# Performance work log

Measured on AMD Instinct MI355X. Metric: run time of the kernel, lower is better.

Reference implementation:

```python
import jax, jax.numpy as jnp
import numpy as np

HEADS = 8
DIM_HEAD = 64
MAX_POS = 512


def setup_inputs() -> dict:
    key = jax.random.key(0)
    ks = jax.random.split(key, 10)
    b, n, dim, inner = 4, 1024, 512, HEADS * DIM_HEAD
    w = lambda k, shape: jax.random.normal(k, shape, jnp.float32) * 0.02
    return {
        "x": jax.random.normal(ks[0], (b, n, dim, 2), jnp.float32),
        "wq_r": w(ks[1], (dim, inner)),
        "wq_i": w(ks[2], (dim, inner)),
        "wkv_r": w(ks[3], (dim, 2 * inner)),
        "wkv_i": w(ks[4], (dim, 2 * inner)),
        "wo_r": w(ks[5], (inner, dim)),
        "wo_i": w(ks[6], (inner, dim)),
        "bo_r": w(ks[7], (dim,)),
        "bo_i": w(ks[8], (dim,)),
        "rel_emb": w(ks[9], (2 * MAX_POS + 1, DIM_HEAD)),
    }


def _clinear(t, Wr, Wi, br=None, bi=None):
    # complex linear: (a+ib)(Wr+iWi) = (aWr - bWi) + i(bWr + aWi)
    a, b = t[..., 0], t[..., 1]
    r = a @ Wr - b @ Wi
    i = b @ Wr + a @ Wi
    if br is not None:
        r = r + br
        i = i + bi
    return jnp.stack((r, i), axis=-1)


def _split_heads(t, h):
    # [b, n, h*d, 2] -> [b, h, n, d, 2]
    b, n, hd, c = t.shape
    return t.reshape(b, n, h, hd // h, c).transpose(0, 2, 1, 3, 4)


def reference(x, wq_r, wq_i, wkv_r, wkv_i, wo_r, wo_i, bo_r, bo_i, rel_emb):
    b, n = x.shape[0], x.shape[1]
    scale = DIM_HEAD ** (-0.5)

    q = _split_heads(_clinear(x, wq_r, wq_i), HEADS)          # [b,h,n,d,2]
    kv = _clinear(x, wkv_r, wkv_i)                            # [b,n,2*inner,2]
    k_, v_ = jnp.split(kv, 2, axis=-2)
    k = _split_heads(k_, HEADS)
    v = _split_heads(v_, HEADS)

    qr, qi = q[..., 0], q[..., 1]
    kr, ki = k[..., 0], k[..., 1]

    dots_r = (jnp.einsum('bhid,bhjd->bhij', qr, kr)
              - jnp.einsum('bhid,bhjd->bhij', qi, ki)) * scale
    dots_i = (jnp.einsum('bhid,bhjd->bhij', qr, ki)
              + jnp.einsum('bhid,bhjd->bhij', qi, kr)) * scale

    seq = jnp.arange(n)
    dist = jnp.clip(seq[:, None] - seq[None, :], -MAX_POS, MAX_POS) + MAX_POS  # [n,n]
    rel = rel_emb[dist]                                       # [n, n, d]
    dots_r = dots_r + jnp.einsum('bhnd,nrd->bhnr', qr, rel) * scale
    dots_i = dots_i + jnp.einsum('bhnd,nrd->bhnr', qi, rel) * scale

    # magnitude softmax over keys
    attn = jax.nn.softmax(jnp.sqrt(dots_r ** 2 + dots_i ** 2), axis=-1)  # [b,h,i,j]

    vr, vi = v[..., 0], v[..., 1]
    out_r = jnp.einsum('bhij,bhjd->bhid', attn, vr)
    out_i = jnp.einsum('bhij,bhjd->bhid', attn, vi)
    # [b,h,n,d] -> [b,n,h*d]
    out_r = out_r.transpose(0, 2, 1, 3).reshape(b, n, -1)
    out_i = out_i.transpose(0, 2, 1, 3).reshape(b, n, -1)
    out = jnp.stack((out_r, out_i), axis=-1)                  # [b,n,inner,2]

    # to_out (with bias); dropout prob 0 -> identity
    return _clinear(out, wo_r, wo_i, bo_r, bo_i)
```

## Files before the change

### kernel.cpp

```cpp
#include <hip/hip_runtime.h>
#include <hip/hip_bf16.h>


using bf16 = __bf16;
typedef __bf16 bf16x8 __attribute__((ext_vector_type(8)));
typedef float f32x4 __attribute__((ext_vector_type(4)));
typedef unsigned u32x4 __attribute__((ext_vector_type(4)));

#define MFMA16(a, b, c) __builtin_amdgcn_mfma_f32_16x16x32_bf16((a), (b), (c), 0, 0, 0)

__device__ __forceinline__ float ld_in(const void* p, long long i, int f32) {
  return f32 ? ((const float*)p)[i] : (float)((const bf16*)p)[i];
}

__device__ __forceinline__ void gl_lds16(const bf16* g, const bf16* l) {
  __builtin_amdgcn_global_load_lds(
      (const __attribute__((address_space(1))) void*)(unsigned long long)g,
      (__attribute__((address_space(3))) void*)(unsigned int)(unsigned long long)l,
      16, 0, 0);
}

template <int CTRL>
__device__ __forceinline__ float dpp_mv(float v) {
  int s = __builtin_bit_cast(int, v);
  return __builtin_bit_cast(float,
      __builtin_amdgcn_update_dpp(s, s, CTRL, 0xf, 0xf, false));
}
__device__ __forceinline__ float dpp_sum16(float v) {
  v += dpp_mv<0x121>(v);
  v += dpp_mv<0x122>(v);
  v += dpp_mv<0x124>(v);
  v += dpp_mv<0x128>(v);
  return v;
}

__device__ __forceinline__ unsigned pack_bf16(float lo, float hi) {
  unsigned a = (unsigned)__builtin_bit_cast(unsigned short, (bf16)lo);
  unsigned b = (unsigned)__builtin_bit_cast(unsigned short, (bf16)hi);
  return a | (b << 16);
}
__device__ __forceinline__ unsigned pack2h(bf16 lo, bf16 hi) {
  unsigned a = (unsigned)__builtin_bit_cast(unsigned short, lo);
  unsigned b = (unsigned)__builtin_bit_cast(unsigned short, hi);
  return a | (b << 16);
}

__global__ __launch_bounds__(256) void k_diag(float* __restrict__ out, float v) {
  int idx = blockIdx.x * 256 + threadIdx.x;
  if (idx < 4194304) out[idx] = v;
}

__global__ void k_detect_all(
    const unsigned short* p0, const unsigned short* p1, const unsigned short* p2,
    const unsigned short* p3, const unsigned short* p4, const unsigned short* p5,
    const unsigned short* p6, const unsigned short* p7, const unsigned short* p8,
    const unsigned short* p9, int* __restrict__ flags) {
  static const int sizes[10] = {65536, 65536, 65536, 65536, 65536,
                                65536, 65536, 512, 512, 65536};
  const unsigned short* ptrs[10] = {p0, p1, p2, p3, p4, p5, p6, p7, p8, p9};
  __shared__ int cnt;
  if (threadIdx.x == 0) cnt = 0;
  __syncthreads();
  const int which = blockIdx.x;
  const unsigned short* p = ptrs[which];
  const int nhalf = sizes[which];
  const int ns = nhalf < 4096 ? nhalf : 4096;
  const int stp = nhalf / ns;
  int c = 0;
  for (int i = threadIdx.x; i < ns; i += 256) {
    const unsigned u = p[(size_t)i * stp];
    const unsigned e = (u >> 7) & 0xFF;
    if (e == 0xFF || (e < 64 && (u & 0x7FFF) != 0)) ++c;
  }
  atomicAdd(&cnt, c);
  __syncthreads();
  if (threadIdx.x == 0) flags[which] = (cnt > (ns >> 6)) ? 1 : 0;
}

__global__ __launch_bounds__(256) void k_build_all(
    const void* __restrict__ x,
    const void* __restrict__ wq_r, const void* __restrict__ wq_i,
    const void* __restrict__ wkv_r, const void* __restrict__ wkv_i,
    const void* __restrict__ wo_r, const void* __restrict__ wo_i,
    const void* __restrict__ rel,
    bf16* __restrict__ wct, bf16* __restrict__ wot,
    bf16* __restrict__ xd, bf16* __restrict__ rel_c,
    const int* __restrict__ flags) {
  __shared__ float tile[64][65];
  const int bid = blockIdx.x;
  const int t = threadIdx.x;
  if (bid < 1024) {
    const bool is_o = bid >= 768;
    const int lb = is_o ? bid - 768 : bid;
    const int k0 = (lb & 15) * 64;
    const int c0 = (lb >> 4) * 64;
    const int kk0 = k0 & 511;
    const bool hi = k0 >= 512;
    const void* src;
    int f, ld, scol;
    float sgn = 1.f;
    if (is_o) {
      ld = 512;
      if (c0 < 512) { scol = c0;       if (!hi) { src = wo_r; f = flags[5]; } else { src = wo_i; f = flags[6]; sgn = -1.f; } }
      else          { scol = c0 - 512; if (!hi) { src = wo_i; f = flags[6]; } else { src = wo_r; f = flags[5]; } }
    } else {
      if (c0 < 512)       { scol = c0;        ld = 512;  if (!hi) { src = wq_r;  f = flags[1]; } else { src = wq_i;  f = flags[2]; sgn = -1.f; } }
      else if (c0 < 1024) { scol = c0 - 512;  ld = 512;  if (!hi) { src = wq_i;  f = flags[2]; } else { src = wq_r;  f = flags[1]; } }
      else if (c0 < 2048) { scol = c0 - 1024; ld = 1024; if (!hi) { src = wkv_r; f = flags[3]; } else { src = wkv_i; f = flags[4]; sgn = -1.f; } }
      else                { scol = c0 - 2048; ld = 1024; if (!hi) { src = wkv_i; f = flags[4]; } else { src = wkv_r; f = flags[3]; } }
    }
    const int cc = t & 63, rq = t >> 6;
#pragma unroll
    for (int rp = 0; rp < 16; ++rp) {
      const int rr = rp * 4 + rq;
      tile[rr][cc] = sgn * ld_in(src, (long long)(kk0 + rr) * ld + scol + cc, f);
    }
    __syncthreads();
    bf16* dst = is_o ? wot : wct;
    const int cr = t >> 3, kb = (t & 7) * 8;
#pragma unroll
    for (int p = 0; p < 2; ++p) {
      const int c = cr + p * 32;
      bf16x8 v;
#pragma unroll
      for (int e = 0; e < 8; ++e) v[e] = (bf16)tile[kb + e][c];
      *(bf16x8*)(dst + (size_t)(c0 + c) * 1024 + k0 + kb) = v;
    }
  } else if (bid < 9216) {
    const int f = flags[0];
    int idx = (bid - 1024) * 256 + t;
    int m = idx >> 9, j = idx & 511;
    long long base = (long long)m * 1024 + j * 2;
    xd[(size_t)m * 1024 + j] = (bf16)ld_in(x, base, f);
    xd[(size_t)m * 1024 + 512 + j] = (bf16)ld_in(x, base + 1, f);
  } else {
    const int f = flags[9];
    int idx = (bid - 9216) * 256 + t;
    if (idx < 65600) rel_c[idx] = (bf16)ld_in(rel, idx, f);
  }
}

template <int MODE, int BN>
__global__ __launch_bounds__(256) void k_gemm(
    const bf16* __restrict__ A, const bf16* __restrict__ Bt,
    bf16* __restrict__ C, float* __restrict__ Cf,
    const int M, const int N, const int K,
    const void* __restrict__ bias_r, const void* __restrict__ bias_i,
    const int* __restrict__ flags) {
  constexpr int MT = (BN == 128) ? 4 : 2;
  __shared__ __align__(16) bf16 As[128 * 32];
  __shared__ __align__(16) bf16 Bs[BN * 32];
  const int tid = threadIdx.x;
  const int wave = tid >> 6, lane = tid & 63;
  const int lane15 = lane & 15, quad = lane >> 4;
  const int qk0 = quad * 8;
  const int per = gridDim.x >> 3;
  const int s = (blockIdx.x & 7) * per + (blockIdx.x >> 3);
  const int nbx = N / BN;
  const int bm = (s / nbx) * 128, bn = (s % nbx) * BN;
  int wm, wn;
  if constexpr (BN == 128) { wm = (wave >> 1) * 64; wn = (wave & 1) * 64; }
  else                     { wm = wave * 32;        wn = 0; }
  const int sr = lane >> 2;
  const int sc = (lane & 3) * 8;
  f32x4 acc[MT][4];
#pragma unroll
  for (int i = 0; i < MT; ++i)
#pragma unroll
    for (int j = 0; j < 4; ++j) acc[i][j] = (f32x4){0.f, 0.f, 0.f, 0.f};

  for (int k0 = 0; k0 < K; k0 += 32) {
#pragma unroll
    for (int p = 0; p < 2; ++p) {
      const int r0 = p * 64 + wave * 16;
      gl_lds16(A + (size_t)(bm + r0 + sr) * K + k0 + sc, As + r0 * 32);
    }
    if constexpr (BN == 128) {
#pragma unroll
      for (int p = 0; p < 2; ++p) {
        const int r0 = p * 64 + wave * 16;
        gl_lds16(Bt + (size_t)(bn + r0 + sr) * K + k0 + sc, Bs + r0 * 32);
      }
    } else {
      const int r0 = wave * 16;
      gl_lds16(Bt + (size_t)(bn + r0 + sr) * K + k0 + sc, Bs + r0 * 32);
    }
    __syncthreads();
    bf16x8 af[MT], bfr[4];
#pragma unroll
    for (int mt = 0; mt < MT; ++mt) af[mt] = *(const bf16x8*)(As + (wm + mt * 16 + lane15) * 32 + qk0);
#pragma unroll
    for (int nt = 0; nt < 4; ++nt) bfr[nt] = *(const bf16x8*)(Bs + (wn + nt * 16 + lane15) * 32 + qk0);
#pragma unroll
    for (int mt = 0; mt < MT; ++mt)
#pragma unroll
      for (int nt = 0; nt < 4; ++nt) acc[mt][nt] = MFMA16(af[mt], bfr[nt], acc[mt][nt]);
    __syncthreads();
  }
  int fbr = 0, fbi = 0;
  if constexpr (MODE == 1) { fbr = flags[7]; fbi = flags[8]; }
#pragma unroll
  for (int mt = 0; mt < MT; ++mt)
#pragma unroll
    for (int nt = 0; nt < 4; ++nt)
#pragma unroll
      for (int r = 0; r < 4; ++r) {
        const int m = bm + wm + mt * 16 + quad * 4 + r;
        const int n = bn + wn + nt * 16 + lane15;
        float v = acc[mt][nt][r];
        if constexpr (MODE == 0) {
          C[(size_t)m * N + n] = (bf16)v;
        } else {
          const int c = (n < 512) ? n : n - 512;
          v += ld_in((n < 512) ? bias_r : bias_i, c, (n < 512) ? fbr : fbi);
          Cf[(size_t)m * 1024 + c * 2 + ((n < 512) ? 0 : 1)] = v;
        }
      }
}

__global__ __launch_bounds__(256) void k_vt(const bf16* __restrict__ C1,
                                            bf16* __restrict__ vt_r, bf16* __restrict__ vt_i) {
  __shared__ __align__(16) bf16 tr[64][72], ti[64][72];
  const int bid = blockIdx.x, tid = threadIdx.x;
  const int bh = bid >> 4, jt = bid & 15;
  const int b = bh >> 3, h = bh & 7;
  const int j0 = jt * 64;
#pragma unroll
  for (int p = 0; p < 2; ++p) {
    const int j = p * 32 + (tid >> 3);
    const int d0 = (tid & 7) * 8;
    const size_t base = (size_t)(b * 1024 + j0 + j) * 3072 + h * 64 + d0;
    *(bf16x8*)&tr[j][d0] = *(const bf16x8*)(C1 + base + 1536);
    *(bf16x8*)&ti[j][d0] = *(const bf16x8*)(C1 + base + 2560);
  }
  __syncthreads();
#pragma unroll
  for (int p = 0; p < 2; ++p) {
    const int d = p * 32 + (tid >> 3);
    const int p0 = (tid & 7) * 4;
    u32x4 wr, wi;
#pragma unroll
    for (int e = 0; e < 4; ++e) {
      const int pp = p0 + e;
      const int j1 = ((pp >> 4) << 5) + (pp & 15);
      wr[e] = pack2h(tr[j1][d], tr[j1 + 16][d]);
      wi[e] = pack2h(ti[j1][d], ti[j1 + 16][d]);
    }
    const size_t dst = (size_t)(bh * 64 + d) * 512 + jt * 32 + p0;
    *(u32x4*)((unsigned*)vt_r + dst) = wr;
    *(u32x4*)((unsigned*)vt_i + dst) = wi;
  }
}

__device__ __forceinline__ bf16x8 lds_frag72(const bf16* base, int row, int kofs) {
  return *(const bf16x8*)(base + row * 72 + kofs);
}

__global__ __launch_bounds__(256, 2) void k_attn(
    const bf16* __restrict__ C1, const bf16* __restrict__ vt_r, const bf16* __restrict__ vt_i,
    const bf16* __restrict__ rel, bf16* __restrict__ Oc) {
  __shared__ __align__(16) bf16 kr_s[64 * 72];
  __shared__ __align__(16) bf16 ki_s[64 * 72];
  __shared__ __align__(16) bf16 vtr_s[64 * 72];
  __shared__ __align__(16) bf16 vti_s[64 * 72];
  __shared__ unsigned Gt32[4][1360];

  const int tid = threadIdx.x;
  const int wave = tid >> 6, lane = tid & 63;
  const int lane15 = lane & 15, quad = lane >> 4;
  const int qk0 = quad * 8;
  const int bid0 = blockIdx.x;
  const int bid = (bid0 & 7) * 64 + (bid0 >> 3);
  const int bh = bid >> 4, it = bid & 15;
  const int b = bh >> 3, h = bh & 7;
  const int i0 = it * 64;
  const int tq = tid >> 3;
  const int tc = (tid & 7) * 8;

  unsigned* const Gw = &Gt32[wave][0];

  const size_t qbase = (size_t)(b * 1024 + i0 + wave * 16 + lane15) * 3072 + h * 64;
  bf16x8 aqr[2], aqi[2], aqin[2];
  aqr[0] = *(const bf16x8*)(C1 + qbase + qk0);
  aqr[1] = *(const bf16x8*)(C1 + qbase + 32 + qk0);
  aqi[0] = *(const bf16x8*)(C1 + qbase + 512 + qk0);
  aqi[1] = *(const bf16x8*)(C1 + qbase + 512 + 32 + qk0);
#pragma unroll
  for (int c = 0; c < 2; ++c)
#pragma unroll
    for (int e = 0; e < 8; ++e) aqin[c][e] = (bf16)(-(float)aqi[c][e]);

  f32x4 o_r[4], o_i[4];
#pragma unroll
  for (int dt = 0; dt < 4; ++dt) { o_r[dt] = (f32x4){0.f,0.f,0.f,0.f}; o_i[dt] = (f32x4){0.f,0.f,0.f,0.f}; }
  f32x4 l_st = (f32x4){0.f, 0.f, 0.f, 0.f};

  bf16x8 pKr[2], pKi[2], pVr[2], pVi[2];
  auto issueKV = [&](int jtn) {
    const int j0 = jtn * 64;
#pragma unroll
    for (int p = 0; p < 2; ++p) {
      const int row = p * 32 + tq;
      const size_t gbase = (size_t)(b * 1024 + j0 + row) * 3072 + h * 64 + tc;
      pKr[p] = *(const bf16x8*)(C1 + gbase + 1024);
      pKi[p] = *(const bf16x8*)(C1 + gbase + 2048);
      const size_t vbase = (size_t)(bh * 64 + row) * 1024 + j0 + tc;
      pVr[p] = *(const bf16x8*)(vt_r + vbase);
      pVi[p] = *(const bf16x8*)(vt_i + vbase);
    }
  };

  bf16x8 rb0[5], rb1[5];
  auto loadR = [&](int jtn) {
    const int t0w = 449 + i0 - jtn * 64 + wave * 16;
#pragma unroll
    for (int g = 0; g < 5; ++g) {
      int trw = t0w + g * 16 + lane15;
      trw = trw < 0 ? 0 : (trw > 1024 ? 1024 : trw);
      const bf16* rp = rel + (size_t)trw * 64;
      rb0[g] = *(const bf16x8*)(rp + qk0);
      rb1[g] = *(const bf16x8*)(rp + 32 + qk0);
    }
  };

  issueKV(0);
  loadR(0);
  for (int jt = 0; jt < 16; ++jt) {
#pragma unroll
    for (int p = 0; p < 2; ++p) {
      const int row = p * 32 + tq;
      *(bf16x8*)(kr_s + row * 72 + tc) = pKr[p];
      *(bf16x8*)(ki_s + row * 72 + tc) = pKi[p];
      *(bf16x8*)(vtr_s + row * 72 + tc) = pVr[p];
      *(bf16x8*)(vti_s + row * 72 + tc) = pVi[p];
    }
    __syncthreads();
    if (jt < 15) issueKV(jt + 1);

#pragma unroll
    for (int g = 0; g < 5; ++g) {
      f32x4 gr = (f32x4){0.f,0.f,0.f,0.f}, gi = (f32x4){0.f,0.f,0.f,0.f};
      gr = MFMA16(aqr[0], rb0[g], gr);
      gr = MFMA16(aqr[1], rb1[g], gr);
      gi = MFMA16(aqi[0], rb0[g], gi);
      gi = MFMA16(aqi[1], rb1[g], gi);
      const int trow = (g * 16 + lane15) * 17;
#pragma unroll
      for (int r = 0; r < 4; ++r)
        Gw[trow + quad * 4 + r] = pack_bf16(gr[r], gi[r]);
    }

    if (jt < 15) loadR(jt + 1);

    f32x4 s_r[4], s_i[4];
#pragma unroll
    for (int ct = 0; ct < 4; ++ct) { s_r[ct] = (f32x4){0.f,0.f,0.f,0.f}; s_i[ct] = (f32x4){0.f,0.f,0.f,0.f}; }
    __builtin_amdgcn_s_setprio(1);
#pragma unroll
    for (int ct = 0; ct < 4; ++ct) {
      const int krow = ct * 16 + lane15;
      bf16x8 bkr0 = lds_frag72(kr_s, krow, qk0), bkr1 = lds_frag72(kr_s, krow, 32 + qk0);
      bf16x8 bki0 = lds_frag72(ki_s, krow, qk0), bki1 = lds_frag72(ki_s, krow, 32 + qk0);
      s_r[ct] = MFMA16(aqr[0], bkr0, s_r[ct]);
      s_r[ct] = MFMA16(aqr[1], bkr1, s_r[ct]);
      s_r[ct] = MFMA16(aqin[0], bki0, s_r[ct]);
      s_r[ct] = MFMA16(aqin[1], bki1, s_r[ct]);
      s_i[ct] = MFMA16(aqr[0], bki0, s_i[ct]);
      s_i[ct] = MFMA16(aqr[1], bki1, s_i[ct]);
      s_i[ct] = MFMA16(aqi[0], bkr0, s_i[ct]);
      s_i[ct] = MFMA16(aqi[1], bkr1, s_i[ct]);
    }
    __builtin_amdgcn_s_setprio(0);

    float mag[4][4];
#pragma unroll
    for (int ct = 0; ct < 4; ++ct) {
      const int jj = ct * 16 + lane15;
#pragma unroll
      for (int r = 0; r < 4; ++r) {
        const int ii = quad * 4 + r;
        const unsigned gv = Gw[(ii - jj + 63) * 17 + ii];
        const float gr = __builtin_bit_cast(float, gv << 16);
        const float gi = __builtin_bit_cast(float, gv & 0xffff0000u);
        const float dr = s_r[ct][r] + gr;
        const float di = s_i[ct][r] + gi;
        mag[ct][r] = fminf(0.125f * sqrtf(dr * dr + di * di), 80.f);
      }
    }

#pragma unroll
    for (int r = 0; r < 4; ++r) {
      const int ii = quad * 4 + r;
      const float p0 = __expf(mag[0][r]), p1 = __expf(mag[1][r]);
      l_st[r] += p0 + p1;
      Gw[ii * 36 + lane15] = pack_bf16(p0, p1);
    }
    bf16x8 ap0 = *(const bf16x8*)((const bf16*)Gw + lane15 * 72 + quad * 8);
    __builtin_amdgcn_s_setprio(1);
#pragma unroll
    for (int dt = 0; dt < 4; ++dt) {
      const int vrow = dt * 16 + lane15;
      o_r[dt] = MFMA16(ap0, lds_frag72(vtr_s, vrow, qk0), o_r[dt]);
      o_i[dt] = MFMA16(ap0, lds_frag72(vti_s, vrow, qk0), o_i[dt]);
    }
    __builtin_amdgcn_s_setprio(0);
#pragma unroll
    for (int r = 0; r < 4; ++r) {
      const int ii = quad * 4 + r;
      const float p2 = __expf(mag[2][r]), p3 = __expf(mag[3][r]);
      l_st[r] += p2 + p3;
      Gw[ii * 36 + 16 + lane15] = pack_bf16(p2, p3);
    }
    bf16x8 ap1 = *(const bf16x8*)((const bf16*)Gw + lane15 * 72 + 32 + quad * 8);
    __builtin_amdgcn_s_setprio(1);
#pragma unroll
    for (int dt = 0; dt < 4; ++dt) {
      const int vrow = dt * 16 + lane15;
      o_r[dt] = MFMA16(ap1, lds_frag72(vtr_s, vrow, 32 + qk0), o_r[dt]);
      o_i[dt] = MFMA16(ap1, lds_frag72(vti_s, vrow, 32 + qk0), o_i[dt]);
    }
    __builtin_amdgcn_s_setprio(0);
    __syncthreads();
  }

  const size_t obase = (size_t)(b * 1024 + i0 + wave * 16) * 1024 + h * 64;
#pragma unroll
  for (int r = 0; r < 4; ++r) {
    const float inv = 1.0f / dpp_sum16(l_st[r]);
    const int ii = quad * 4 + r;
#pragma unroll
    for (int dt = 0; dt < 4; ++dt) {
      Oc[obase + (size_t)ii * 1024 + dt * 16 + lane15] = (bf16)(o_r[dt][r] * inv);
      Oc[obase + (size_t)ii * 1024 + 512 + dt * 16 + lane15] = (bf16)(o_i[dt][r] * inv);
    }
  }
}

extern "C" void kernel_launch(void* const* d_in, const int* in_sizes, int n_in,
                              void* d_out, int out_size, void* d_ws, size_t ws_size,
                              hipStream_t stream) {
  float* out = (float*)d_out;

  if (n_in != 10) { k_diag<<<16384, 256, 0, stream>>>(out, 300000.f); return; }
  if (out_size != 4194304) { k_diag<<<16384, 256, 0, stream>>>(out, 400000.f); return; }
  static const int dict_sizes[10] = {4194304, 262144, 262144, 524288, 524288,
                                     262144, 262144, 512, 512, 65600};
  for (int i = 0; i < 10; ++i) {
    if (in_sizes[i] != dict_sizes[i]) { k_diag<<<16384, 256, 0, stream>>>(out, 200000.f); return; }
  }
  const size_t NEED = 50462888;
  if (ws_size < NEED) { k_diag<<<16384, 256, 0, stream>>>(out, 100000.f); return; }

  const void* x     = d_in[0];
  const void* wq_r  = d_in[1];
  const void* wq_i  = d_in[2];
  const void* wkv_r = d_in[3];
  const void* wkv_i = d_in[4];
  const void* wo_r  = d_in[5];
  const void* wo_i  = d_in[6];
  const void* bo_r  = d_in[7];
  const void* bo_i  = d_in[8];
  const void* rel   = d_in[9];

  char* ws = (char*)d_ws;
  bf16* C1   = (bf16*)(ws);
  bf16* Xd   = (bf16*)(ws + 25165824);
  bf16* Vtr  = (bf16*)(ws + 25165824);
  bf16* Vti  = (bf16*)(ws + 29360128);
  bf16* Oc   = (bf16*)(ws + 33554432);
  bf16* WcT  = (bf16*)(ws + 41943040);
  bf16* WoT  = (bf16*)(ws + 48234496);
  bf16* relc = (bf16*)(ws + 50331648);
  int*  flags= (int*)(ws + 50462848);

  k_detect_all<<<10, 256, 0, stream>>>(
      (const unsigned short*)x, (const unsigned short*)wq_r, (const unsigned short*)wq_i,
      (const unsigned short*)wkv_r, (const unsigned short*)wkv_i, (const unsigned short*)wo_r,
      (const unsigned short*)wo_i, (const unsigned short*)bo_r, (const unsigned short*)bo_i,
      (const unsigned short*)rel, flags);

  k_build_all<<<9473, 256, 0, stream>>>(x, wq_r, wq_i, wkv_r, wkv_i, wo_r, wo_i, rel,
                                        WcT, WoT, Xd, relc, flags);

  k_gemm<0, 128><<<768, 256, 0, stream>>>(Xd, WcT, C1, nullptr, 4096, 3072, 1024,
                                          nullptr, nullptr, flags);
  k_vt<<<512, 256, 0, stream>>>(C1, Vtr, Vti);
  k_attn<<<512, 256, 0, stream>>>(C1, Vtr, Vti, relc, Oc);
  k_gemm<1, 64><<<512, 256, 0, stream>>>(Oc, WoT, nullptr, out, 4096, 1024, 1024,
                                         bo_r, bo_i, flags);
}
```

Before: 231.7 us.

## Split attention key tiles across wave pairs and load V fragments directly from global

The attention kernel now gives each block 32 query rows instead of 64 and runs 1024 blocks. Two waves share each 16-row query group and each takes half of every 64-key tile, with their partial outputs and row sums combined through shared memory at the end. The V transpose kernel writes V in MFMA fragment order, so attention reads V fragments straight from global memory instead of staging them in LDS. This cuts LDS use and the relative-position work per wave, aiming at more resident blocks and parallelism. The cost is twice the Q/K traffic across blocks, an extra barrier per tile, and a final cross-wave reduction.

```diff
diff --git a/kernel.cpp b/kernel.cpp
--- a/kernel.cpp
+++ b/kernel.cpp
@@ -234,21 +234,21 @@
     *(bf16x8*)&ti[j][d0] = *(const bf16x8*)(C1 + base + 2560);
   }
   __syncthreads();
-#pragma unroll
-  for (int p = 0; p < 2; ++p) {
-    const int d = p * 32 + (tid >> 3);
-    const int p0 = (tid & 7) * 4;
+  const int dt = tid >> 6, l = tid & 63;
+  const int q = l >> 4, m = l & 15;
+  const int d = dt * 16 + m;
+  const size_t base = ((size_t)(bh * 16 + jt) << 11) + (size_t)dt * 512 + l * 4;
+#pragma unroll
+  for (int half = 0; half < 2; ++half) {
     u32x4 wr, wi;
 #pragma unroll
     for (int e = 0; e < 4; ++e) {
-      const int pp = p0 + e;
-      const int j1 = ((pp >> 4) << 5) + (pp & 15);
+      const int j1 = half * 32 + q * 4 + e;
       wr[e] = pack2h(tr[j1][d], tr[j1 + 16][d]);
       wi[e] = pack2h(ti[j1][d], ti[j1 + 16][d]);
     }
-    const size_t dst = (size_t)(bh * 64 + d) * 512 + jt * 32 + p0;
-    *(u32x4*)((unsigned*)vt_r + dst) = wr;
-    *(u32x4*)((unsigned*)vt_i + dst) = wi;
+    *(u32x4*)((unsigned*)vt_r + base + half * 256) = wr;
+    *(u32x4*)((unsigned*)vt_i + base + half * 256) = wi;
   }
 }
 
@@ -256,30 +256,31 @@
   return *(const bf16x8*)(base + row * 72 + kofs);
 }
 
-__global__ __launch_bounds__(256, 2) void k_attn(
+__global__ __launch_bounds__(256) void k_attn(
     const bf16* __restrict__ C1, const bf16* __restrict__ vt_r, const bf16* __restrict__ vt_i,
     const bf16* __restrict__ rel, bf16* __restrict__ Oc) {
-  __shared__ __align__(16) bf16 kr_s[64 * 72];
-  __shared__ __align__(16) bf16 ki_s[64 * 72];
-  __shared__ __align__(16) bf16 vtr_s[64 * 72];
-  __shared__ __align__(16) bf16 vti_s[64 * 72];
-  __shared__ unsigned Gt32[4][1360];
+  __shared__ __align__(16) bf16 k_s[2][64 * 72];
+  __shared__ __align__(16) unsigned Gt32[4][816];
 
   const int tid = threadIdx.x;
   const int wave = tid >> 6, lane = tid & 63;
+  const int wq = wave >> 1;
+  const int jh = wave & 1;
   const int lane15 = lane & 15, quad = lane >> 4;
   const int qk0 = quad * 8;
   const int bid0 = blockIdx.x;
-  const int bid = (bid0 & 7) * 64 + (bid0 >> 3);
-  const int bh = bid >> 4, it = bid & 15;
+  const int bid = (bid0 & 7) * 128 + (bid0 >> 3);
+  const int bh = bid >> 5, qt = bid & 31;
   const int b = bh >> 3, h = bh & 7;
-  const int i0 = it * 64;
+  const int i0 = qt * 32;
   const int tq = tid >> 3;
   const int tc = (tid & 7) * 8;
 
   unsigned* const Gw = &Gt32[wave][0];
-
-  const size_t qbase = (size_t)(b * 1024 + i0 + wave * 16 + lane15) * 3072 + h * 64;
+  bf16* const krs = &k_s[0][0];
+  bf16* const kis = &k_s[1][0];
+
+  const size_t qbase = (size_t)(b * 1024 + i0 + wq * 16 + lane15) * 3072 + h * 64;
   bf16x8 aqr[2], aqi[2], aqin[2];
   aqr[0] = *(const bf16x8*)(C1 + qbase + qk0);
   aqr[1] = *(const bf16x8*)(C1 + qbase + 32 + qk0);
@@ -295,8 +296,8 @@
   for (int dt = 0; dt < 4; ++dt) { o_r[dt] = (f32x4){0.f,0.f,0.f,0.f}; o_i[dt] = (f32x4){0.f,0.f,0.f,0.f}; }
   f32x4 l_st = (f32x4){0.f, 0.f, 0.f, 0.f};
 
-  bf16x8 pKr[2], pKi[2], pVr[2], pVi[2];
-  auto issueKV = [&](int jtn) {
+  bf16x8 pKr[2], pKi[2];
+  auto issueK = [&](int jtn) {
     const int j0 = jtn * 64;
 #pragma unroll
     for (int p = 0; p < 2; ++p) {
@@ -304,18 +305,15 @@
       const size_t gbase = (size_t)(b * 1024 + j0 + row) * 3072 + h * 64 + tc;
       pKr[p] = *(const bf16x8*)(C1 + gbase + 1024);
       pKi[p] = *(const bf16x8*)(C1 + gbase + 2048);
-      const size_t vbase = (size_t)(bh * 64 + row) * 1024 + j0 + tc;
-      pVr[p] = *(const bf16x8*)(vt_r + vbase);
-      pVi[p] = *(const bf16x8*)(vt_i + vbase);
     }
   };
 
-  bf16x8 rb0[5], rb1[5];
+  bf16x8 rb0[3], rb1[3];
   auto loadR = [&](int jtn) {
-    const int t0w = 449 + i0 - jtn * 64 + wave * 16;
-#pragma unroll
-    for (int g = 0; g < 5; ++g) {
-      int trw = t0w + g * 16 + lane15;
+    const int t0g = 449 + i0 - jtn * 64 + wq * 16 + (jh ? 0 : 32);
+#pragma unroll
+    for (int g = 0; g < 3; ++g) {
+      int trw = t0g + g * 16 + lane15;
       trw = trw < 0 ? 0 : (trw > 1024 ? 1024 : trw);
       const bf16* rp = rel + (size_t)trw * 64;
       rb0[g] = *(const bf16x8*)(rp + qk0);
@@ -323,22 +321,20 @@
     }
   };
 
-  issueKV(0);
+  issueK(0);
   loadR(0);
   for (int jt = 0; jt < 16; ++jt) {
 #pragma unroll
     for (int p = 0; p < 2; ++p) {
       const int row = p * 32 + tq;
-      *(bf16x8*)(kr_s + row * 72 + tc) = pKr[p];
-      *(bf16x8*)(ki_s + row * 72 + tc) = pKi[p];
-      *(bf16x8*)(vtr_s + row * 72 + tc) = pVr[p];
-      *(bf16x8*)(vti_s + row * 72 + tc) = pVi[p];
+      *(bf16x8*)(krs + row * 72 + tc) = pKr[p];
+      *(bf16x8*)(kis + row * 72 + tc) = pKi[p];
     }
     __syncthreads();
-    if (jt < 15) issueKV(jt + 1);
-
-#pragma unroll
-    for (int g = 0; g < 5; ++g) {
+    if (jt < 15) issueK(jt + 1);
+
+#pragma unroll
+    for (int g = 0; g < 3; ++g) {
       f32x4 gr = (f32x4){0.f,0.f,0.f,0.f}, gi = (f32x4){0.f,0.f,0.f,0.f};
       gr = MFMA16(aqr[0], rb0[g], gr);
       gr = MFMA16(aqr[1], rb1[g], gr);
@@ -349,89 +345,98 @@
       for (int r = 0; r < 4; ++r)
         Gw[trow + quad * 4 + r] = pack_bf16(gr[r], gi[r]);
     }
-
     if (jt < 15) loadR(jt + 1);
 
-    f32x4 s_r[4], s_i[4];
-#pragma unroll
-    for (int ct = 0; ct < 4; ++ct) { s_r[ct] = (f32x4){0.f,0.f,0.f,0.f}; s_i[ct] = (f32x4){0.f,0.f,0.f,0.f}; }
+    f32x4 s_r[2], s_i[2];
+#pragma unroll
+    for (int c = 0; c < 2; ++c) { s_r[c] = (f32x4){0.f,0.f,0.f,0.f}; s_i[c] = (f32x4){0.f,0.f,0.f,0.f}; }
     __builtin_amdgcn_s_setprio(1);
 #pragma unroll
-    for (int ct = 0; ct < 4; ++ct) {
-      const int krow = ct * 16 + lane15;
-      bf16x8 bkr0 = lds_frag72(kr_s, krow, qk0), bkr1 = lds_frag72(kr_s, krow, 32 + qk0);
-      bf16x8 bki0 = lds_frag72(ki_s, krow, qk0), bki1 = lds_frag72(ki_s, krow, 32 + qk0);
-      s_r[ct] = MFMA16(aqr[0], bkr0, s_r[ct]);
-      s_r[ct] = MFMA16(aqr[1], bkr1, s_r[ct]);
-      s_r[ct] = MFMA16(aqin[0], bki0, s_r[ct]);
-      s_r[ct] = MFMA16(aqin[1], bki1, s_r[ct]);
-      s_i[ct] = MFMA16(aqr[0], bki0, s_i[ct]);
-      s_i[ct] = MFMA16(aqr[1], bki1, s_i[ct]);
-      s_i[ct] = MFMA16(aqi[0], bkr0, s_i[ct]);
-      s_i[ct] = MFMA16(aqi[1], bkr1, s_i[ct]);
+    for (int ctl = 0; ctl < 2; ++ctl) {
+      const int krow = (jh * 2 + ctl) * 16 + lane15;
+      bf16x8 bkr0 = lds_frag72(krs, krow, qk0), bkr1 = lds_frag72(krs, krow, 32 + qk0);
+      bf16x8 bki0 = lds_frag72(kis, krow, qk0), bki1 = lds_frag72(kis, krow, 32 + qk0);
+      s_r[ctl] = MFMA16(aqr[0], bkr0, s_r[ctl]);
+      s_r[ctl] = MFMA16(aqr[1], bkr1, s_r[ctl]);
+      s_r[ctl] = MFMA16(aqin[0], bki0, s_r[ctl]);
+      s_r[ctl] = MFMA16(aqin[1], bki1, s_r[ctl]);
+      s_i[ctl] = MFMA16(aqr[0], bki0, s_i[ctl]);
+      s_i[ctl] = MFMA16(aqr[1], bki1, s_i[ctl]);
+      s_i[ctl] = MFMA16(aqi[0], bkr0, s_i[ctl]);
+      s_i[ctl] = MFMA16(aqi[1], bkr1, s_i[ctl]);
     }
     __builtin_amdgcn_s_setprio(0);
-
-    float mag[4][4];
-#pragma unroll
-    for (int ct = 0; ct < 4; ++ct) {
-      const int jj = ct * 16 + lane15;
+    __syncthreads();
+
+    const unsigned* vbr = (const unsigned*)vt_r + (((size_t)(bh * 16 + jt)) << 11) + jh * 256;
+    const unsigned* vbi = (const unsigned*)vt_i + (((size_t)(bh * 16 + jt)) << 11) + jh * 256;
+    bf16x8 vrf[4];
+#pragma unroll
+    for (int dt = 0; dt < 4; ++dt) vrf[dt] = *(const bf16x8*)(vbr + dt * 512 + lane * 4);
+
+    float mag[2][4];
+#pragma unroll
+    for (int ctl = 0; ctl < 2; ++ctl) {
+      const int jjl = ctl * 16 + lane15;
 #pragma unroll
       for (int r = 0; r < 4; ++r) {
         const int ii = quad * 4 + r;
-        const unsigned gv = Gw[(ii - jj + 63) * 17 + ii];
+        const unsigned gv = Gw[(ii - jjl + 31) * 17 + ii];
         const float gr = __builtin_bit_cast(float, gv << 16);
         const float gi = __builtin_bit_cast(float, gv & 0xffff0000u);
-        const float dr = s_r[ct][r] + gr;
-        const float di = s_i[ct][r] + gi;
-        mag[ct][r] = fminf(0.125f * sqrtf(dr * dr + di * di), 80.f);
+        const float dr = s_r[ctl][r] + gr;
+        const float di = s_i[ctl][r] + gi;
+        mag[ctl][r] = fminf(0.125f * sqrtf(dr * dr + di * di), 80.f);
       }
     }
-
 #pragma unroll
     for (int r = 0; r < 4; ++r) {
       const int ii = quad * 4 + r;
       const float p0 = __expf(mag[0][r]), p1 = __expf(mag[1][r]);
       l_st[r] += p0 + p1;
-      Gw[ii * 36 + lane15] = pack_bf16(p0, p1);
-    }
-    bf16x8 ap0 = *(const bf16x8*)((const bf16*)Gw + lane15 * 72 + quad * 8);
+      Gw[ii * 18 + lane15] = pack_bf16(p0, p1);
+    }
+    bf16x8 vif[4];
+#pragma unroll
+    for (int dt = 0; dt < 4; ++dt) vif[dt] = *(const bf16x8*)(vbi + dt * 512 + lane * 4);
+
+    bf16x8 ap = *(const bf16x8*)((const bf16*)Gw + lane15 * 36 + quad * 8);
     __builtin_amdgcn_s_setprio(1);
 #pragma unroll
+    for (int dt = 0; dt < 4; ++dt) o_r[dt] = MFMA16(ap, vrf[dt], o_r[dt]);
+#pragma unroll
+    for (int dt = 0; dt < 4; ++dt) o_i[dt] = MFMA16(ap, vif[dt], o_i[dt]);
+    __builtin_amdgcn_s_setprio(0);
+  }
+
+  float* cb = (float*)&k_s[0][0];
+  const int cidx = (wq * 64 + lane) * 36;
+  if (jh == 1) {
+#pragma unroll
     for (int dt = 0; dt < 4; ++dt) {
-      const int vrow = dt * 16 + lane15;
-      o_r[dt] = MFMA16(ap0, lds_frag72(vtr_s, vrow, qk0), o_r[dt]);
-      o_i[dt] = MFMA16(ap0, lds_frag72(vti_s, vrow, qk0), o_i[dt]);
-    }
-    __builtin_amdgcn_s_setprio(0);
+      *(f32x4*)(cb + cidx + dt * 8) = o_r[dt];
+      *(f32x4*)(cb + cidx + dt * 8 + 4) = o_i[dt];
+    }
+    *(f32x4*)(cb + cidx + 32) = l_st;
+  }
+  __syncthreads();
+  if (jh == 0) {
+#pragma unroll
+    for (int dt = 0; dt < 4; ++dt) {
+      o_r[dt] += *(const f32x4*)(cb + cidx + dt * 8);
+      o_i[dt] += *(const f32x4*)(cb + cidx + dt * 8 + 4);
+    }
+    l_st += *(const f32x4*)(cb + cidx + 32);
+    const size_t obase = (size_t)(b * 1024 + i0 + wq * 16) * 1024 + h * 64;
 #pragma unroll
     for (int r = 0; r < 4; ++r) {
+      const float inv = 1.0f / dpp_sum16(l_st[r]);
       const int ii = quad * 4 + r;
-      const float p2 = __expf(mag[2][r]), p3 = __expf(mag[3][r]);
-      l_st[r] += p2 + p3;
-      Gw[ii * 36 + 16 + lane15] = pack_bf16(p2, p3);
-    }
-    bf16x8 ap1 = *(const bf16x8*)((const bf16*)Gw + lane15 * 72 + 32 + quad * 8);
-    __builtin_amdgcn_s_setprio(1);
-#pragma unroll
-    for (int dt = 0; dt < 4; ++dt) {
-      const int vrow = dt * 16 + lane15;
-      o_r[dt] = MFMA16(ap1, lds_frag72(vtr_s, vrow, 32 + qk0), o_r[dt]);
-      o_i[dt] = MFMA16(ap1, lds_frag72(vti_s, vrow, 32 + qk0), o_i[dt]);
-    }
-    __builtin_amdgcn_s_setprio(0);
-    __syncthreads();
-  }
-
-  const size_t obase = (size_t)(b * 1024 + i0 + wave * 16) * 1024 + h * 64;
-#pragma unroll
-  for (int r = 0; r < 4; ++r) {
-    const float inv = 1.0f / dpp_sum16(l_st[r]);
-    const int ii = quad * 4 + r;
-#pragma unroll
-    for (int dt = 0; dt < 4; ++dt) {
-      Oc[obase + (size_t)ii * 1024 + dt * 16 + lane15] = (bf16)(o_r[dt][r] * inv);
-      Oc[obase + (size_t)ii * 1024 + 512 + dt * 16 + lane15] = (bf16)(o_i[dt][r] * inv);
+#pragma unroll
+      for (int dt = 0; dt < 4; ++dt) {
+        Oc[obase + (size_t)ii * 1024 + dt * 16 + lane15] = (bf16)(o_r[dt][r] * inv);
+        Oc[obase + (size_t)ii * 1024 + 512 + dt * 16 + lane15] = (bf16)(o_i[dt][r] * inv);
+      }
     }
   }
 }
@@ -485,7 +490,7 @@
   k_gemm<0, 128><<<768, 256, 0, stream>>>(Xd, WcT, C1, nullptr, 4096, 3072, 1024,
                                           nullptr, nullptr, flags);
   k_vt<<<512, 256, 0, stream>>>(C1, Vtr, Vti);
-  k_attn<<<512, 256, 0, stream>>>(C1, Vtr, Vti, relc, Oc);
+  k_attn<<<1024, 256, 0, stream>>>(C1, Vtr, Vti, relc, Oc);
   k_gemm<1, 64><<<512, 256, 0, stream>>>(Oc, WoT, nullptr, out, 4096, 1024, 1024,
                                          bo_r, bo_i, flags);
 }
```

After: 240.2 us. 3.7% more time.
